# Performance work log

Measured on AMD Instinct MI355X. Metric: run time of the kernel, lower is better.

The kernel has to match this reference:

```python
import jax, jax.numpy as jnp
import numpy as np

N = 100000       # num nodes
E = 3200000      # train message edges (avg degree 32)
EP = 1600000     # pos (and neg) decode edges
F_IN = 128       # node feature dim
H1, H2 = 50, 10  # GCN layer widths from source


def setup_inputs() -> dict:
    key = jax.random.key(0)
    ks = jax.random.split(key, 6)
    x = jax.random.normal(ks[0], (N, F_IN), dtype=jnp.float32)
    train_pos_edge_index = jax.random.randint(ks[1], (2, E), 0, N)
    pos_edge_index = jax.random.randint(ks[2], (2, EP), 0, N)
    neg_edge_index = jax.random.randint(ks[3], (2, EP), 0, N)
    W1 = jax.random.normal(ks[4], (F_IN, H1), dtype=jnp.float32) / np.float32(np.sqrt(F_IN))
    b1 = jnp.zeros((H1,), jnp.float32)
    W2 = jax.random.normal(ks[5], (H1, H2), dtype=jnp.float32) / np.float32(np.sqrt(H1))
    b2 = jnp.zeros((H2,), jnp.float32)
    return {"x": x, "W1": W1, "b1": b1, "W2": W2, "b2": b2,
            "train_pos_edge_index": train_pos_edge_index,
            "pos_edge_index": pos_edge_index,
            "neg_edge_index": neg_edge_index}


def gcn_conv(x, W, b, src, dst, num_nodes):
    # x: [N, Fin] -> transform first (PyG GCNConv), then normalize+aggregate.
    h = x @ W                                                        # [N, Fout]
    deg = jax.ops.segment_sum(jnp.ones(src.shape, h.dtype), dst,
                              num_segments=num_nodes)                # in-degree incl self-loops
    dinv = jnp.where(deg > 0, jax.lax.rsqrt(deg), 0.0)
    norm = dinv[src] * dinv[dst]                                     # [E']
    msgs = h[src] * norm[:, None]                                    # gather + scale
    out = jax.ops.segment_sum(msgs, dst, num_segments=num_nodes)     # scatter-add
    return out + b


def reference(x, W1, b1, W2, b2, train_pos_edge_index, pos_edge_index, neg_edge_index):
    # GCNConv adds self-loops to the message edge set.
    loops = jnp.arange(N, dtype=train_pos_edge_index.dtype)
    src = jnp.concatenate([train_pos_edge_index[0], loops])
    dst = jnp.concatenate([train_pos_edge_index[1], loops])
    # encode(): conv1 -> relu -> conv2
    h = jax.nn.relu(gcn_conv(x, W1, b1, src, dst, N))                # [N, 50]
    z = gcn_conv(h, W2, b2, src, dst, N)                             # [N, 10]
    # decode(): concat pos/neg edges, edge-wise dot product of endpoint embeddings
    ei = jnp.concatenate([pos_edge_index, neg_edge_index], axis=-1)  # [2, 2*EP]
    logits = jnp.sum(z[ei[0]] * z[ei[1]], axis=-1)                   # [2*EP]
    return logits
```

## Files before the change

### kernel.cpp

```cpp
#include <hip/hip_runtime.h>

#define FIN 128
#define H1_ 50
#define H2_ 10
#define ST2S 16

#define BKT_SHIFT 7
#define BKT_W 128
#define NB_MAX 800
#define SB_SHIFT 11
#define SB_W 2048
#define NSB_MAX 64
#define SB_CAP 81920
#define P1_CHUNK 8192
#define P1F_CHUNK 4096
#define SCH 16


__device__ inline float bf2f(unsigned int u16) {
    union { unsigned int i; float f; } c; c.i = u16 << 16; return c.f;
}
__device__ inline unsigned short f2bf(float f) {
    union { float f; unsigned int i; } c; c.f = f;
    unsigned int x = c.i;
    return (unsigned short)((x + 0x7FFFu + ((x >> 16) & 1u)) >> 16);
}


__global__ __launch_bounds__(256) void partition_sb(const int* __restrict__ src,
                                                    const int* __restrict__ dst,
                                                    int* __restrict__ sbcnt,
                                                    int* __restrict__ bcnt,
                                                    int* __restrict__ pairbuf1,
                                                    int E, int nsb) {
    __shared__ int lh[NB_MAX];
    __shared__ int lhs[NSB_MAX];
    __shared__ int lbs[NSB_MAX];
    int tid = threadIdx.x;
    for (int i = tid; i < NB_MAX; i += 256) lh[i] = 0;
    if (tid < NSB_MAX) lhs[tid] = 0;
    __syncthreads();
    int lo = blockIdx.x * P1_CHUNK;
    int hi = min(lo + P1_CHUNK, E);
    for (int e = lo + tid; e < hi; e += 256)
        atomicAdd(&lh[dst[e] >> BKT_SHIFT], 1);
    __syncthreads();
    if (tid < nsb) {
        int c = 0;
#pragma unroll
        for (int j = 0; j < 16; ++j) {
            int idx = tid * 16 + j;
            c += (idx < NB_MAX) ? lh[idx] : 0;
        }
        lbs[tid] = c ? (tid * SB_CAP + atomicAdd(&sbcnt[tid], c)) : 0;
    }
    for (int i = tid; i < NB_MAX; i += 256) {
        int c = lh[i];
        if (c) atomicAdd(&bcnt[i], c);
    }
    __syncthreads();
    for (int e = lo + tid; e < hi; e += 256) {
        int sv = src[e], d = dst[e];
        int b = d >> SB_SHIFT;
        int r = atomicAdd(&lhs[b], 1);
        pairbuf1[lbs[b] + r] = sv | ((d & (SB_W - 1)) << 17);
    }
}

__global__ __launch_bounds__(256) void bucket_scan(const int* __restrict__ bcnt,
                                                   int* __restrict__ bbase,
                                                   int* __restrict__ bcursor,
                                                   int nb2, int E) {
    __shared__ int s[256];
    int t = threadIdx.x;
    int base = t * 4;
    int v0 = (base + 0 < nb2) ? bcnt[base + 0] : 0;
    int v1 = (base + 1 < nb2) ? bcnt[base + 1] : 0;
    int v2 = (base + 2 < nb2) ? bcnt[base + 2] : 0;
    int v3 = (base + 3 < nb2) ? bcnt[base + 3] : 0;
    int tsum = v0 + v1 + v2 + v3;
    s[t] = tsum;
    __syncthreads();
    for (int off = 1; off < 256; off <<= 1) {
        int x = (t >= off) ? s[t - off] : 0;
        __syncthreads();
        s[t] += x;
        __syncthreads();
    }
    int excl = s[t] - tsum;
    if (t == 0) bbase[nb2] = E;
    if (base + 0 < nb2) { bbase[base + 0] = excl; bcursor[base + 0] = excl; }
    excl += v0;
    if (base + 1 < nb2) { bbase[base + 1] = excl; bcursor[base + 1] = excl; }
    excl += v1;
    if (base + 2 < nb2) { bbase[base + 2] = excl; bcursor[base + 2] = excl; }
    excl += v2;
    if (base + 3 < nb2) { bbase[base + 3] = excl; bcursor[base + 3] = excl; }
}


__global__ __launch_bounds__(256) void partition_fine(const int* __restrict__ pairbuf1,
                                                      const int* __restrict__ sbcnt,
                                                      int* __restrict__ bcursor,
                                                      int* __restrict__ pairbuf2) {
    int sb = blockIdx.y;
    int cnt = sbcnt[sb];
    int rel = blockIdx.x * P1F_CHUNK;
    if (rel >= cnt) return;
    int lo = sb * SB_CAP + rel;
    int hi = sb * SB_CAP + min(rel + P1F_CHUNK, cnt);
    __shared__ int lh[16];
    __shared__ int lb[16];
    int tid = threadIdx.x;
    if (tid < 16) lh[tid] = 0;
    __syncthreads();
    for (int j = lo + tid; j < hi; j += 256)
        atomicAdd(&lh[(pairbuf1[j] >> 17) >> BKT_SHIFT], 1);
    __syncthreads();
    if (tid < 16) {
        int c = lh[tid];
        lb[tid] = c ? atomicAdd(&bcursor[sb * 16 + tid], c) : 0;
        lh[tid] = 0;
    }
    __syncthreads();
    for (int j = lo + tid; j < hi; j += 256) {
        int p = pairbuf1[j];
        int din = p >> 17;
        int fb = din >> BKT_SHIFT;
        int r = atomicAdd(&lh[fb], 1);
        pairbuf2[lb[fb] + r] = (p & 0x1FFFF) | ((din & (BKT_W - 1)) << 17);
    }
}


__global__ __launch_bounds__(256) void bucket_fill_scan(const int* __restrict__ pairbuf,
                                                        const int* __restrict__ bbase,
                                                        int* __restrict__ rowptr,
                                                        float* __restrict__ dinv,
                                                        int* __restrict__ ecol,
                                                        int N, int E) {
    __shared__ int cnt2[BKT_W * SCH];
    __shared__ int sc[BKT_W];
    int b = blockIdx.x;
    int base_node = b << BKT_SHIFT;
    int nnodes = min(BKT_W, N - base_node);
    int tid = threadIdx.x;
    for (int i = tid; i < BKT_W * SCH; i += 256) cnt2[i] = 0;
    __syncthreads();
    int lo = bbase[b], hi = bbase[b + 1];
    for (int j = lo + tid; j < hi; j += 256) {
        int p = pairbuf[j];
        atomicAdd(&cnt2[(p >> 17) * SCH + ((p & 0x1FFFF) >> 13)], 1);
    }
    __syncthreads();
    int tsum = 0;
    if (tid < BKT_W) {
#pragma unroll
        for (int c = 0; c < SCH; ++c) tsum += cnt2[tid * SCH + c];
        sc[tid] = tsum;
    }
    __syncthreads();
    for (int off = 1; off < BKT_W; off <<= 1) {
        int xv = (tid >= off && tid < BKT_W) ? sc[tid - off] : 0;
        __syncthreads();
        if (tid < BKT_W) sc[tid] += xv;
        __syncthreads();
    }
    if (tid < nnodes) {
        int rp = lo + sc[tid] - tsum;
        rowptr[base_node + tid] = rp;
        dinv[base_node + tid] = rsqrtf(1.0f + (float)tsum);
        int run = rp;
#pragma unroll
        for (int c = 0; c < SCH; ++c) {
            int v = cnt2[tid * SCH + c];
            cnt2[tid * SCH + c] = run;
            run += v;
        }
    }
    __syncthreads();
    for (int j = lo + tid; j < hi; j += 256) {
        int p = pairbuf[j];
        int s = p & 0x1FFFF;
        int pos = atomicAdd(&cnt2[(p >> 17) * SCH + (s >> 13)], 1);
        ecol[pos] = s;
    }
    if (b == (int)gridDim.x - 1 && tid == 0) rowptr[N] = E;
}


#define G1_NODES 128
#define SX_PITCH 132
#define KCHUNK 32
__global__ __launch_bounds__(256) void gemm1_kernel(const float* __restrict__ x,
                                                    const float* __restrict__ W1,
                                                    const float* __restrict__ dinv,
                                                    unsigned short* __restrict__ st1p, int N) {
    __shared__ float sX[G1_NODES * SX_PITCH];
    __shared__ float sW[KCHUNK * 64];
    int tid = threadIdx.x;
    int nb = blockIdx.x * G1_NODES;
    {
        const float4* x4 = (const float4*)(x + (size_t)nb * FIN);
        for (int i = tid; i < G1_NODES * 32; i += 256) {
            int ln = i >> 5, kk = i & 31;
            float4 v = (nb + ln < N) ? x4[(size_t)ln * 32 + kk]
                                     : make_float4(0.f, 0.f, 0.f, 0.f);
            *(float4*)(&sX[ln * SX_PITCH + kk * 4]) = v;
        }
    }
    int q = tid >> 3;
    int g = tid & 7;
    const float* xr0 = &sX[(4 * q + 0) * SX_PITCH];
    const float* xr1 = &sX[(4 * q + 1) * SX_PITCH];
    const float* xr2 = &sX[(4 * q + 2) * SX_PITCH];
    const float* xr3 = &sX[(4 * q + 3) * SX_PITCH];
    float acc[4][8];
#pragma unroll
    for (int i = 0; i < 4; ++i)
#pragma unroll
        for (int j = 0; j < 8; ++j) acc[i][j] = 0.0f;

    for (int kc = 0; kc < FIN / KCHUNK; ++kc) {
        __syncthreads();
        for (int i = tid; i < KCHUNK * 64; i += 256) {
            int k = i >> 6, f = i & 63;
            sW[i] = (f < H1_) ? W1[(kc * KCHUNK + k) * H1_ + f] : 0.0f;
        }
        __syncthreads();
        int kb = kc * KCHUNK;
#pragma unroll 4
        for (int k = 0; k < KCHUNK; ++k) {
            float xv0 = xr0[kb + k];
            float xv1 = xr1[kb + k];
            float xv2 = xr2[kb + k];
            float xv3 = xr3[kb + k];
            const float* w = &sW[k * 64 + g * 8];
#pragma unroll
            for (int j = 0; j < 8; ++j) {
                float wv = w[j];
                acc[0][j] = fmaf(xv0, wv, acc[0][j]);
                acc[1][j] = fmaf(xv1, wv, acc[1][j]);
                acc[2][j] = fmaf(xv2, wv, acc[2][j]);
                acc[3][j] = fmaf(xv3, wv, acc[3][j]);
            }
        }
    }
#pragma unroll
    for (int i = 0; i < 4; ++i) {
        int node = nb + 4 * q + i;
        if (node >= N) continue;
        if (g == 7) continue;
        float di = dinv[node];
        unsigned short o[8];
#pragma unroll
        for (int j = 0; j < 8; ++j) o[j] = f2bf(acc[i][j] * di);
        uint4 pk;
        pk.x = (unsigned)o[0] | ((unsigned)o[1] << 16);
        pk.y = (unsigned)o[2] | ((unsigned)o[3] << 16);
        pk.z = (unsigned)o[4] | ((unsigned)o[5] << 16);
        pk.w = (unsigned)o[6] | ((unsigned)o[7] << 16);
        *(uint4*)(st1p + (size_t)node * 64 + g * 8) = pk;
    }
}


#define F2 25
__global__ __launch_bounds__(256) void csr_aggregate1(const unsigned short* __restrict__ st,
                                                      const int* __restrict__ rowptr,
                                                      const int* __restrict__ ecol,
                                                      const float* __restrict__ dinv,
                                                      const float* __restrict__ b,
                                                      float* __restrict__ out, int N) {
    int idx = blockIdx.x * blockDim.x + threadIdx.x;
    if (idx >= N * F2) return;
    int d  = idx / F2;
    int fp = idx - d * F2;
    int fo = 2 * fp;
    unsigned int self2 = *(const unsigned int*)(st + (size_t)d * 64 + fo);
    float acc0 = bf2f(self2 & 0xFFFFu);
    float acc1 = bf2f(self2 >> 16);
    int j = rowptr[d], end = rowptr[d + 1];
    for (; j + 3 < end; j += 4) {
        int s0 = ecol[j], s1 = ecol[j + 1], s2 = ecol[j + 2], s3 = ecol[j + 3];
        unsigned int v0 = *(const unsigned int*)(st + (size_t)s0 * 64 + fo);
        unsigned int v1 = *(const unsigned int*)(st + (size_t)s1 * 64 + fo);
        unsigned int v2 = *(const unsigned int*)(st + (size_t)s2 * 64 + fo);
        unsigned int v3 = *(const unsigned int*)(st + (size_t)s3 * 64 + fo);
        acc0 += (bf2f(v0 & 0xFFFFu) + bf2f(v1 & 0xFFFFu)) + (bf2f(v2 & 0xFFFFu) + bf2f(v3 & 0xFFFFu));
        acc1 += (bf2f(v0 >> 16) + bf2f(v1 >> 16)) + (bf2f(v2 >> 16) + bf2f(v3 >> 16));
    }
    for (; j < end; ++j) {
        unsigned int v = *(const unsigned int*)(st + (size_t)ecol[j] * 64 + fo);
        acc0 += bf2f(v & 0xFFFFu);
        acc1 += bf2f(v >> 16);
    }
    float vd = dinv[d];
    float r0 = fmaxf(fmaf(vd, acc0, b[fo]),     0.0f);
    float r1 = fmaxf(fmaf(vd, acc1, b[fo + 1]), 0.0f);
    *(float2*)(out + (size_t)d * H1_ + fo) = make_float2(r0, r1);
}


__global__ __launch_bounds__(256) void gemm2_kernel(const float* __restrict__ h,
                                                    const float* __restrict__ W2,
                                                    const float* __restrict__ dinv,
                                                    float* __restrict__ st2, int n16) {
    __shared__ float sW[H1_ * H2_];
    int tid = threadIdx.x;
    for (int i = tid; i < H1_ * H2_; i += 256) sW[i] = W2[i];
    __syncthreads();
    int idx = blockIdx.x * blockDim.x + tid;
    if (idx >= n16) return;
    int node = idx >> 4;
    int f    = idx & 15;
    if (f >= H2_) { st2[idx] = 0.0f; return; }
    const float* hr = &h[(size_t)node * H1_];
    float acc = 0.0f;
#pragma unroll
    for (int k = 0; k < H1_; ++k) acc = fmaf(hr[k], sW[k * H2_ + f], acc);
    st2[idx] = acc * dinv[node];
}


__global__ __launch_bounds__(256) void csr_aggregate2(const float* __restrict__ st,
                                                      const int* __restrict__ rowptr,
                                                      const int* __restrict__ ecol,
                                                      const float* __restrict__ dinv,
                                                      const float* __restrict__ b,
                                                      float* __restrict__ z0,
                                                      float* __restrict__ z1, int N) {
    int idx = blockIdx.x * blockDim.x + threadIdx.x;
    if (idx >= N * 4) return;
    int d = idx >> 2;
    int g = idx & 3;
    if (g == 3) return;
    const float* row = st + g * 4;
    float4 acc = *(const float4*)(row + (size_t)d * ST2S);
    int j = rowptr[d], end = rowptr[d + 1];
    for (; j + 3 < end; j += 4) {
        int s0 = ecol[j], s1 = ecol[j + 1], s2 = ecol[j + 2], s3 = ecol[j + 3];
        float4 a0 = *(const float4*)(row + (size_t)s0 * ST2S);
        float4 a1 = *(const float4*)(row + (size_t)s1 * ST2S);
        float4 a2 = *(const float4*)(row + (size_t)s2 * ST2S);
        float4 a3 = *(const float4*)(row + (size_t)s3 * ST2S);
        acc.x += (a0.x + a1.x) + (a2.x + a3.x);
        acc.y += (a0.y + a1.y) + (a2.y + a3.y);
        acc.z += (a0.z + a1.z) + (a2.z + a3.z);
        acc.w += (a0.w + a1.w) + (a2.w + a3.w);
    }
    for (; j < end; ++j) {
        float4 a = *(const float4*)(row + (size_t)ecol[j] * ST2S);
        acc.x += a.x; acc.y += a.y; acc.z += a.z; acc.w += a.w;
    }
    float vd = dinv[d];
    if (g < 2) {
        float4 r;
        r.x = fmaf(vd, acc.x, b[4 * g + 0]);
        r.y = fmaf(vd, acc.y, b[4 * g + 1]);
        r.z = fmaf(vd, acc.z, b[4 * g + 2]);
        r.w = fmaf(vd, acc.w, b[4 * g + 3]);
        *(float4*)(z0 + (size_t)d * 8 + 4 * g) = r;
    } else {
        float2 r;
        r.x = fmaf(vd, acc.x, b[8]);
        r.y = fmaf(vd, acc.y, b[9]);
        *(float2*)(z1 + (size_t)d * 2) = r;
    }
}


__global__ __launch_bounds__(256) void decode_kernel(const float* __restrict__ z0,
                                                     const float* __restrict__ z1,
                                                     const int* __restrict__ pos,
                                                     const int* __restrict__ neg,
                                                     float* __restrict__ logits, int EP) {
    int i = blockIdx.x * blockDim.x + threadIdx.x;
    if (i >= 2 * EP) return;
    int a, b;
    if (i < EP) {
        a = __builtin_nontemporal_load(&pos[i]);
        b = __builtin_nontemporal_load(&pos[EP + i]);
    } else {
        int j = i - EP;
        a = __builtin_nontemporal_load(&neg[j]);
        b = __builtin_nontemporal_load(&neg[EP + j]);
    }
    const float4* za = (const float4*)(z0 + (size_t)a * 8);
    const float4* zb = (const float4*)(z0 + (size_t)b * 8);
    float4 a0 = za[0];
    float4 a1 = za[1];
    float4 b0 = zb[0];
    float4 b1 = zb[1];
    float2 a2 = *(const float2*)(z1 + (size_t)a * 2);
    float2 b2 = *(const float2*)(z1 + (size_t)b * 2);
    float acc = a0.x * b0.x;
    acc = fmaf(a0.y, b0.y, acc);
    acc = fmaf(a0.z, b0.z, acc);
    acc = fmaf(a0.w, b0.w, acc);
    acc = fmaf(a1.x, b1.x, acc);
    acc = fmaf(a1.y, b1.y, acc);
    acc = fmaf(a1.z, b1.z, acc);
    acc = fmaf(a1.w, b1.w, acc);
    acc = fmaf(a2.x, b2.x, acc);
    acc = fmaf(a2.y, b2.y, acc);
    __builtin_nontemporal_store(acc, &logits[i]);
}


extern "C" void kernel_launch(void* const* d_in, const int* in_sizes, int n_in,
                              void* d_out, int out_size, void* d_ws, size_t ws_size,
                              hipStream_t stream) {
    const float* x   = (const float*)d_in[0];
    const float* W1  = (const float*)d_in[1];
    const float* b1  = (const float*)d_in[2];
    const float* W2  = (const float*)d_in[3];
    const float* b2  = (const float*)d_in[4];
    const int* train = (const int*)d_in[5];
    const int* pos   = (const int*)d_in[6];
    const int* neg   = (const int*)d_in[7];

    const int N  = in_sizes[0] / FIN;
    const int E  = in_sizes[5] / 2;
    const int EP = in_sizes[6] / 2;

    const int* tsrc = train;
    const int* tdst = train + E;

    size_t off = 0;
    int* rowptr   = (int*)d_ws;              off += (size_t)N + 1;
    int* bcnt     = (int*)d_ws + off;        off += NB_MAX;
    int* sbcnt    = (int*)d_ws + off;        off += NSB_MAX;
    int* bbase    = (int*)d_ws + off;        off += NB_MAX + 1;
    int* bcursor  = (int*)d_ws + off;        off += NB_MAX;
    float* dinv   = (float*)d_ws + off;      off += N;
    off = (off + 15) & ~(size_t)15;
    float* regA   = (float*)d_ws + off;      off += (size_t)32 * N;
    float* regB   = (float*)d_ws + off;
    int* pairbuf2 = (int*)regA;
    unsigned short* st1p = (unsigned short*)regA;
    float* st2    = regA;
    float* z0     = regA + (size_t)16 * N;
    float* z1     = regA + (size_t)24 * N;
    int* pairbuf1 = (int*)regB;
    float* out1   = regB;
    int* ecol     = (int*)d_out;
    float* logits = (float*)d_out;

    const int NB2 = (N + BKT_W - 1) >> BKT_SHIFT;
    const int NSB = (N + SB_W - 1) >> SB_SHIFT;
    const int P1B = (E + P1_CHUNK - 1) / P1_CHUNK;
    const int P1FB = (SB_CAP + P1F_CHUNK - 1) / P1F_CHUNK;

    hipMemsetAsync(bcnt, 0, (NB_MAX + NSB_MAX) * sizeof(int), stream);
    partition_sb<<<P1B, 256, 0, stream>>>(tsrc, tdst, sbcnt, bcnt, pairbuf1, E, NSB);
    bucket_scan<<<1, 256, 0, stream>>>(bcnt, bbase, bcursor, NB2, E);
    partition_fine<<<dim3(P1FB, NSB), 256, 0, stream>>>(pairbuf1, sbcnt, bcursor, pairbuf2);
    bucket_fill_scan<<<NB2, 256, 0, stream>>>(pairbuf2, bbase, rowptr, dinv, ecol, N, E);

    gemm1_kernel<<<(N + G1_NODES - 1) / G1_NODES, 256, 0, stream>>>(x, W1, dinv, st1p, N);
    csr_aggregate1<<<(N * F2 + 255) / 256, 256, 0, stream>>>(
        st1p, rowptr, ecol, dinv, b1, out1, N);

    gemm2_kernel<<<(N * 16 + 255) / 256, 256, 0, stream>>>(out1, W2, dinv, st2, N * 16);
    csr_aggregate2<<<(N * 4 + 255) / 256, 256, 0, stream>>>(
        st2, rowptr, ecol, dinv, b2, z0, z1, N);

    decode_kernel<<<(2 * EP + 255) / 256, 256, 0, stream>>>(z0, z1, pos, neg, logits, EP);
}
```

Measured before the change: 457.8 us.

## Split layer-1 feature table into two 64-byte halves and aggregate per half-row

The GEMM1 output is stored as two separate 64-byte-per-node bf16 tables (features 0-23 and 24-49) instead of one 128-byte-pitch table. The aggregation kernel now uses two threads per node, each gathering a full half-row with wide uint4 loads per neighbor, instead of 25 threads each loading 4 bytes. This is meant to cut the number of scattered load instructions and make each gather touch contiguous 64-byte segments. In exchange, parallelism drops sharply (2 threads per node), register pressure rises with 26 accumulators, and the two halves do unequal work.

```diff
diff --git a/kernel.cpp b/kernel.cpp
--- a/kernel.cpp
+++ b/kernel.cpp
@@ -24,6 +24,12 @@
     union { float f; unsigned int i; } c; c.f = f;
     unsigned int x = c.i;
     return (unsigned short)((x + 0x7FFFu + ((x >> 16) & 1u)) >> 16);
+}
+__device__ inline void unpack8(uint4 v, float* f) {
+    f[0] = bf2f(v.x & 0xFFFFu); f[1] = bf2f(v.x >> 16);
+    f[2] = bf2f(v.y & 0xFFFFu); f[3] = bf2f(v.y >> 16);
+    f[4] = bf2f(v.z & 0xFFFFu); f[5] = bf2f(v.z >> 16);
+    f[6] = bf2f(v.w & 0xFFFFu); f[7] = bf2f(v.w >> 16);
 }
 
 
@@ -195,7 +201,8 @@
 __global__ __launch_bounds__(256) void gemm1_kernel(const float* __restrict__ x,
                                                     const float* __restrict__ W1,
                                                     const float* __restrict__ dinv,
-                                                    unsigned short* __restrict__ st1p, int N) {
+                                                    unsigned short* __restrict__ tabA,
+                                                    unsigned short* __restrict__ tabB, int N) {
     __shared__ float sX[G1_NODES * SX_PITCH];
     __shared__ float sW[KCHUNK * 64];
     int tid = threadIdx.x;
@@ -255,50 +262,88 @@
         unsigned short o[8];
 #pragma unroll
         for (int j = 0; j < 8; ++j) o[j] = f2bf(acc[i][j] * di);
+        if (g == 6) {
+            *(unsigned int*)(tabB + (size_t)node * 32 + 24) =
+                (unsigned)o[0] | ((unsigned)o[1] << 16);
+            continue;
+        }
         uint4 pk;
         pk.x = (unsigned)o[0] | ((unsigned)o[1] << 16);
         pk.y = (unsigned)o[2] | ((unsigned)o[3] << 16);
         pk.z = (unsigned)o[4] | ((unsigned)o[5] << 16);
         pk.w = (unsigned)o[6] | ((unsigned)o[7] << 16);
-        *(uint4*)(st1p + (size_t)node * 64 + g * 8) = pk;
-    }
-}
-
-
-#define F2 25
-__global__ __launch_bounds__(256) void csr_aggregate1(const unsigned short* __restrict__ st,
+        if (g < 3) *(uint4*)(tabA + (size_t)node * 32 + g * 8) = pk;
+        else       *(uint4*)(tabB + (size_t)node * 32 + (g - 3) * 8) = pk;
+    }
+}
+
+
+__global__ __launch_bounds__(256) void csr_aggregate1(const unsigned short* __restrict__ tabA,
+                                                      const unsigned short* __restrict__ tabB,
                                                       const int* __restrict__ rowptr,
                                                       const int* __restrict__ ecol,
                                                       const float* __restrict__ dinv,
                                                       const float* __restrict__ b,
                                                       float* __restrict__ out, int N) {
     int idx = blockIdx.x * blockDim.x + threadIdx.x;
-    if (idx >= N * F2) return;
-    int d  = idx / F2;
-    int fp = idx - d * F2;
-    int fo = 2 * fp;
-    unsigned int self2 = *(const unsigned int*)(st + (size_t)d * 64 + fo);
-    float acc0 = bf2f(self2 & 0xFFFFu);
-    float acc1 = bf2f(self2 >> 16);
+    if (idx >= N * 2) return;
+    int d = idx >> 1;
+    int g = idx & 1;
+    const unsigned short* tab = g ? tabB : tabA;
+    float acc[26];
+    {
+        const uint4* sr = (const uint4*)(tab + (size_t)d * 32);
+        uint4 s0 = sr[0], s1 = sr[1], s2 = sr[2];
+        unpack8(s0, acc); unpack8(s1, acc + 8); unpack8(s2, acc + 16);
+        if (g) {
+            unsigned int se = *(const unsigned int*)(tab + (size_t)d * 32 + 24);
+            acc[24] = bf2f(se & 0xFFFFu); acc[25] = bf2f(se >> 16);
+        } else { acc[24] = 0.0f; acc[25] = 0.0f; }
+    }
     int j = rowptr[d], end = rowptr[d + 1];
-    for (; j + 3 < end; j += 4) {
-        int s0 = ecol[j], s1 = ecol[j + 1], s2 = ecol[j + 2], s3 = ecol[j + 3];
-        unsigned int v0 = *(const unsigned int*)(st + (size_t)s0 * 64 + fo);
-        unsigned int v1 = *(const unsigned int*)(st + (size_t)s1 * 64 + fo);
-        unsigned int v2 = *(const unsigned int*)(st + (size_t)s2 * 64 + fo);
-        unsigned int v3 = *(const unsigned int*)(st + (size_t)s3 * 64 + fo);
-        acc0 += (bf2f(v0 & 0xFFFFu) + bf2f(v1 & 0xFFFFu)) + (bf2f(v2 & 0xFFFFu) + bf2f(v3 & 0xFFFFu));
-        acc1 += (bf2f(v0 >> 16) + bf2f(v1 >> 16)) + (bf2f(v2 >> 16) + bf2f(v3 >> 16));
-    }
-    for (; j < end; ++j) {
-        unsigned int v = *(const unsigned int*)(st + (size_t)ecol[j] * 64 + fo);
-        acc0 += bf2f(v & 0xFFFFu);
-        acc1 += bf2f(v >> 16);
+    for (; j + 1 < end; j += 2) {
+        int sA = ecol[j], sB = ecol[j + 1];
+        const uint4* ra = (const uint4*)(tab + (size_t)sA * 32);
+        const uint4* rb = (const uint4*)(tab + (size_t)sB * 32);
+        uint4 a0 = ra[0], a1 = ra[1], a2 = ra[2];
+        uint4 b0 = rb[0], b1 = rb[1], b2 = rb[2];
+        float fa[24], fbv[24];
+        unpack8(a0, fa); unpack8(a1, fa + 8); unpack8(a2, fa + 16);
+        unpack8(b0, fbv); unpack8(b1, fbv + 8); unpack8(b2, fbv + 16);
+#pragma unroll
+        for (int k = 0; k < 24; ++k) acc[k] += fa[k] + fbv[k];
+        if (g) {
+            unsigned int ea = *(const unsigned int*)(tab + (size_t)sA * 32 + 24);
+            unsigned int eb = *(const unsigned int*)(tab + (size_t)sB * 32 + 24);
+            acc[24] += bf2f(ea & 0xFFFFu) + bf2f(eb & 0xFFFFu);
+            acc[25] += bf2f(ea >> 16) + bf2f(eb >> 16);
+        }
+    }
+    if (j < end) {
+        int s = ecol[j];
+        const uint4* ra = (const uint4*)(tab + (size_t)s * 32);
+        uint4 a0 = ra[0], a1 = ra[1], a2 = ra[2];
+        float fa[24];
+        unpack8(a0, fa); unpack8(a1, fa + 8); unpack8(a2, fa + 16);
+#pragma unroll
+        for (int k = 0; k < 24; ++k) acc[k] += fa[k];
+        if (g) {
+            unsigned int ea = *(const unsigned int*)(tab + (size_t)s * 32 + 24);
+            acc[24] += bf2f(ea & 0xFFFFu);
+            acc[25] += bf2f(ea >> 16);
+        }
     }
     float vd = dinv[d];
-    float r0 = fmaxf(fmaf(vd, acc0, b[fo]),     0.0f);
-    float r1 = fmaxf(fmaf(vd, acc1, b[fo + 1]), 0.0f);
-    *(float2*)(out + (size_t)d * H1_ + fo) = make_float2(r0, r1);
+    int fb0 = g * 24;
+    float* op = out + (size_t)d * H1_ + fb0;
+    int npair = g ? 13 : 12;
+#pragma unroll
+    for (int k = 0; k < 13; ++k) {
+        if (k >= npair) break;
+        float r0 = fmaxf(fmaf(vd, acc[2 * k],     b[fb0 + 2 * k]),     0.0f);
+        float r1 = fmaxf(fmaf(vd, acc[2 * k + 1], b[fb0 + 2 * k + 1]), 0.0f);
+        *(float2*)(op + 2 * k) = make_float2(r0, r1);
+    }
 }
 
 
@@ -438,7 +483,8 @@
     float* regA   = (float*)d_ws + off;      off += (size_t)32 * N;
     float* regB   = (float*)d_ws + off;
     int* pairbuf2 = (int*)regA;
-    unsigned short* st1p = (unsigned short*)regA;
+    unsigned short* tabA = (unsigned short*)regA;
+    unsigned short* tabB = tabA + (size_t)32 * N;
     float* st2    = regA;
     float* z0     = regA + (size_t)16 * N;
     float* z1     = regA + (size_t)24 * N;
@@ -458,9 +504,9 @@
     partition_fine<<<dim3(P1FB, NSB), 256, 0, stream>>>(pairbuf1, sbcnt, bcursor, pairbuf2);
     bucket_fill_scan<<<NB2, 256, 0, stream>>>(pairbuf2, bbase, rowptr, dinv, ecol, N, E);
 
-    gemm1_kernel<<<(N + G1_NODES - 1) / G1_NODES, 256, 0, stream>>>(x, W1, dinv, st1p, N);
-    csr_aggregate1<<<(N * F2 + 255) / 256, 256, 0, stream>>>(
-        st1p, rowptr, ecol, dinv, b1, out1, N);
+    gemm1_kernel<<<(N + G1_NODES - 1) / G1_NODES, 256, 0, stream>>>(x, W1, dinv, tabA, tabB, N);
+    csr_aggregate1<<<(N * 2 + 255) / 256, 256, 0, stream>>>(
+        tabA, tabB, rowptr, ecol, dinv, b1, out1, N);
 
     gemm2_kernel<<<(N * 16 + 255) / 256, 256, 0, stream>>>(out1, W2, dinv, st2, N * 16);
     csr_aggregate2<<<(N * 4 + 255) / 256, 256, 0, stream>>>(
```

After: 500.6 us. 9.3% more time.
